# Performance work log

Measured on AMD Instinct MI355X. Metric: run time of the kernel, lower is better.

Reference implementation:

```python
import jax, jax.numpy as jnp
import numpy as np

N_NODES = 50000
N_EDGES = 800000
D_IN = 128
D_OUT = 128


def setup_inputs() -> dict:
    key = jax.random.key(0)
    ks = jax.random.split(key, 10)
    x = jax.random.normal(ks[0], (N_NODES, D_IN), dtype=jnp.float32)
    src = jax.random.randint(ks[1], (N_EDGES,), 0, N_NODES, dtype=jnp.int32)
    dst = jax.random.randint(ks[2], (N_EDGES,), 0, N_NODES, dtype=jnp.int32)
    s = 1.0 / np.sqrt(D_IN)
    def lin(k, din, dout):
        kw, kb = jax.random.split(k)
        W = jax.random.uniform(kw, (din, dout), minval=-s, maxval=s, dtype=jnp.float32)
        b = jax.random.uniform(kb, (dout,), minval=-s, maxval=s, dtype=jnp.float32)
        return W, b
    W1, b1 = lin(ks[3], D_IN, D_IN)
    W2, b2 = lin(ks[4], D_IN, D_IN)
    W3, b3 = lin(ks[5], D_IN, D_OUT)
    return dict(x=x, W1=W1, b1=b1, W2=W2, b2=b2, W3=W3, b3=b3, src=src, dst=dst)


def reference(x, W1, b1, W2, b2, W3, b3, src, dst):
    n = x.shape[0]
    ones = jnp.ones(src.shape[0], dtype=x.dtype)
    in_deg = jax.ops.segment_sum(ones, dst, num_segments=n)    # [N]
    out_deg = jax.ops.segment_sum(ones, src, num_segments=n)   # [N]

    def sage_gcn(h, W, b):
        # DGL SAGEConv(aggregator_type='gcn'), eval mode (feat_drop = identity):
        # h_neigh = (sum_{j in N(i)} h_j + h_i) / (in_deg_i + 1); out = h_neigh @ W + b
        neigh = jax.ops.segment_sum(h[src], dst, num_segments=n)  # [N, D]
        h_neigh = (neigh + h) / (in_deg + 1.0)[:, None]
        return h_neigh @ W + b

    h = sage_gcn(x, W1, b1)
    h = sage_gcn(h, W2, b2)

    # DGL GraphConv norm='both', allow_zero_in_degree=True:
    # out = D_in^{-1/2} A D_out^{-1/2} h W + b, degrees clamped to >= 1
    norm_out = jnp.clip(out_deg, 1.0) ** -0.5
    norm_in = jnp.clip(in_deg, 1.0) ** -0.5
    hs = h * norm_out[:, None]
    agg = jax.ops.segment_sum(hs[src], dst, num_segments=n)
    out = (agg * norm_in[:, None]) @ W3 + b3
    return out
```

## Files before the change

kernel.cpp:

```cpp
#include <hip/hip_runtime.h>

#define NN 50000
#define NE 800000
#define D 128

#define CH 32
#define EPC (NE / CH)
#define RGH 4
#define NPRH (NN / RGH)
#define CSRCAP (NE + 16 * NN)

typedef short bf16x8 __attribute__((ext_vector_type(8)));
typedef float f32x4 __attribute__((ext_vector_type(4)));


__device__ __forceinline__ unsigned bf16rne(float f) {
  unsigned u = __float_as_uint(f);
  return (u + 0x7fffu + ((u >> 16) & 1u)) >> 16;
}
__device__ __forceinline__ unsigned packbf(float lo, float hi) {
  return bf16rne(lo) | (bf16rne(hi) << 16);
}

__global__ __launch_bounds__(256) void cvtw_kernel(const float* __restrict__ x,
                                                   const float* __restrict__ W1,
                                                   const float* __restrict__ W2,
                                                   const float* __restrict__ W3,
                                                   unsigned short* __restrict__ hbf,
                                                   unsigned short* __restrict__ T1,
                                                   unsigned short* __restrict__ T2,
                                                   unsigned short* __restrict__ T3) {
  int b = blockIdx.x;
  int tid = threadIdx.x;
  if (b < 6250) {
    int i = b * 256 + tid;
    float4 v = ((const float4*)x)[i];
    uint2 p;
    p.x = packbf(v.x, v.y);
    p.y = packbf(v.z, v.w);
    ((uint2*)hbf)[i] = p;
  } else if (b < 6442) {
    int g = b - 6250;
    int w = g >> 6;
    int i = (g & 63) * 256 + tid;
    const float* W = (w == 0) ? W1 : (w == 1) ? W2 : W3;
    unsigned short* T = (w == 0) ? T1 : (w == 1) ? T2 : T3;
    int n = i >> 7, k = i & 127;
    T[n * 128 + k] = (unsigned short)bf16rne(W[k * 128 + n]);
  } else {
    if (tid < 16) ((uint4*)(hbf + (size_t)NN * D))[tid] = make_uint4(0, 0, 0, 0);
  }
}

__global__ __launch_bounds__(1024) void hist_kernel(const int* __restrict__ src,
                                                    const int* __restrict__ dst,
                                                    int* __restrict__ partial_dst,
                                                    int* __restrict__ partial_src) {
  __shared__ int hd[NPRH];
  __shared__ int hs[NPRH];
  int tid = threadIdx.x;
  int c = blockIdx.x >> 2;
  int r = blockIdx.x & 3;
  int base = r * NPRH;
  for (int i = tid; i < NPRH; i += 1024) { hd[i] = 0; hs[i] = 0; }
  __syncthreads();
  int e0 = c * EPC;
  for (int i = tid; i < EPC; i += 1024) {
    int d = dst[e0 + i];
    int s = src[e0 + i];
    unsigned dr = (unsigned)(d - base);
    unsigned sr = (unsigned)(s - base);
    if (dr < NPRH) atomicAdd(&hd[dr], 1);
    if (sr < NPRH) atomicAdd(&hs[sr], 1);
  }
  __syncthreads();
  for (int i = tid; i < NPRH; i += 1024) {
    partial_dst[c * NN + base + i] = hd[i];
    partial_src[c * NN + base + i] = hs[i];
  }
}

__device__ __forceinline__ int block_excl_scan(int v, int* wsum) {
  int lane = threadIdx.x & 63;
  int w = threadIdx.x >> 6;
  int incl = v;
#pragma unroll
  for (int off = 1; off < 64; off <<= 1) {
    int t = __shfl_up(incl, off);
    if (lane >= off) incl += t;
  }
  if (lane == 63) wsum[w] = incl;
  __syncthreads();
  int wo = 0;
#pragma unroll
  for (int j = 0; j < 4; ++j)
    if (j < w) wo += wsum[j];
  return wo + incl - v;
}

__global__ __launch_bounds__(256) void degscan_kernel(int* __restrict__ partial_dst,
                                                      const int* __restrict__ partial_src,
                                                      int* __restrict__ degtmp,
                                                      int* __restrict__ deg_out,
                                                      int* __restrict__ row_ptr,
                                                      int* __restrict__ partials, int N) {
  __shared__ int wsum[4];
  int d = blockIdx.x * 256 + threadIdx.x;
  int run = 0;
  if (d < N) {
#pragma unroll
    for (int c = 0; c < CH; ++c) {
      int v = partial_dst[c * NN + d];
      partial_dst[c * NN + d] = run;
      run += v;
    }
    degtmp[d] = run;
    int ro = 0;
#pragma unroll
    for (int c = 0; c < CH; ++c) ro += partial_src[c * NN + d];
    deg_out[d] = ro;
  }
  int pad = (run + 15) & ~15;
  int excl = block_excl_scan(pad, wsum);
  if (d < N) row_ptr[d] = excl;
  if (threadIdx.x == 255) partials[blockIdx.x] = excl + pad;
}

__global__ __launch_bounds__(256) void scan2(int* __restrict__ partials,
                                             int* __restrict__ row_ptr, int nb, int N) {
  __shared__ int wsum[4];
  int v = (threadIdx.x < nb) ? partials[threadIdx.x] : 0;
  int excl = block_excl_scan(v, wsum);
  if (threadIdx.x < nb) partials[threadIdx.x] = excl;
  if (threadIdx.x == nb - 1) row_ptr[N] = excl + v;
}

__global__ __launch_bounds__(256) void scan3(int* __restrict__ row_ptr,
                                             const int* __restrict__ partials, int N) {
  int i = blockIdx.x * 256 + threadIdx.x;
  if (i < N) row_ptr[i] += partials[blockIdx.x];
}

__global__ __launch_bounds__(1024) void fill_kernel(const int* __restrict__ src,
                                                    const int* __restrict__ dst,
                                                    const int* __restrict__ row_ptr,
                                                    const int* __restrict__ partial_dst,
                                                    int* __restrict__ csr_src) {
  __shared__ int cur[NPRH];
  int tid = threadIdx.x;
  int c = blockIdx.x >> 2;
  int r = blockIdx.x & 3;
  int base = r * NPRH;
  for (int i = tid; i < NPRH; i += 1024)
    cur[i] = row_ptr[base + i] + partial_dst[c * NN + base + i];
  __syncthreads();
  int e0 = c * EPC;
  for (int i = tid; i < EPC; i += 1024) {
    int d = dst[e0 + i];
    unsigned dr = (unsigned)(d - base);
    if (dr < NPRH) {
      int pos = atomicAdd(&cur[dr], 1);
      csr_src[pos] = src[e0 + i];
    }
  }
}

__global__ __launch_bounds__(256) void pad_kernel(const int* __restrict__ row_ptr,
                                                  const int* __restrict__ degtmp,
                                                  int* __restrict__ csr_src, int N) {
  int i = blockIdx.x * 256 + threadIdx.x;
  if (i >= N) return;
  int s = row_ptr[i] + degtmp[i];
  int e = row_ptr[i + 1];
  for (int j = s; j < e; ++j) csr_src[j] = NN;
}

__device__ __forceinline__ void bacc(float* a, uint4 u) {
  a[0] += __uint_as_float(u.x << 16);
  a[1] += __uint_as_float(u.x & 0xffff0000u);
  a[2] += __uint_as_float(u.y << 16);
  a[3] += __uint_as_float(u.y & 0xffff0000u);
  a[4] += __uint_as_float(u.z << 16);
  a[5] += __uint_as_float(u.z & 0xffff0000u);
  a[6] += __uint_as_float(u.w << 16);
  a[7] += __uint_as_float(u.w & 0xffff0000u);
}

template <int MODE>
__global__ __launch_bounds__(256, 8) void agg_kernel(const unsigned short* __restrict__ hb,
                                                     const int* __restrict__ row_ptr,
                                                     const int* __restrict__ csr_src,
                                                     const int* __restrict__ degtmp,
                                                     unsigned short* __restrict__ outb, int N) {
  int wid = blockIdx.x * 4 + (threadIdx.x >> 6);
  int lane = threadIdx.x & 63;
  if (wid >= N) return;
  int start = row_ptr[wid];
  int iters = (row_ptr[wid + 1] - start) >> 4;
  int indeg = degtmp[wid];
  int q = lane >> 4;
  int col = lane & 15;
  uint4 sr = make_uint4(0, 0, 0, 0);
  if (MODE == 0) sr = ((const uint4*)(hb + (size_t)wid * D))[col];
  float a0[8] = {0, 0, 0, 0, 0, 0, 0, 0};
  float a1[8] = {0, 0, 0, 0, 0, 0, 0, 0};
  const int* ce = csr_src + start + q;
  for (int it = 0; it < iters; ++it, ce += 16) {
    int i0 = ce[0];
    int i1 = ce[4];
    int i2 = ce[8];
    int i3 = ce[12];
    uint4 u0 = ((const uint4*)(hb + (size_t)i0 * D))[col];
    uint4 u1 = ((const uint4*)(hb + (size_t)i1 * D))[col];
    uint4 u2 = ((const uint4*)(hb + (size_t)i2 * D))[col];
    uint4 u3 = ((const uint4*)(hb + (size_t)i3 * D))[col];
    bacc(a0, u0);
    bacc(a1, u1);
    bacc(a0, u2);
    bacc(a1, u3);
  }
#pragma unroll
  for (int j = 0; j < 8; ++j) a0[j] += a1[j];
#pragma unroll
  for (int j = 0; j < 8; ++j) {
    a0[j] += __shfl_xor(a0[j], 16);
    a0[j] += __shfl_xor(a0[j], 32);
  }
  if (MODE == 0) {
    float sf[8] = {0, 0, 0, 0, 0, 0, 0, 0};
    bacc(sf, sr);
    float inv = 1.0f / (float)(indeg + 1);
#pragma unroll
    for (int j = 0; j < 8; ++j) a0[j] = (a0[j] + sf[j]) * inv;
  } else {
    float sc = rsqrtf(fmaxf((float)indeg, 1.0f));
#pragma unroll
    for (int j = 0; j < 8; ++j) a0[j] *= sc;
  }
  if (q == 0) {
    uint4 p;
    p.x = packbf(a0[0], a0[1]);
    p.y = packbf(a0[2], a0[3]);
    p.z = packbf(a0[4], a0[5]);
    p.w = packbf(a0[6], a0[7]);
    ((uint4*)(outb + (size_t)wid * D))[col] = p;
  }
}

template <int MODE, int OUT_BF>
__global__ __launch_bounds__(256) void mgemm_kernel(const unsigned short* __restrict__ A,
                                                    const unsigned short* __restrict__ WT,
                                                    const float* __restrict__ bias,
                                                    const int* __restrict__ deg_out,
                                                    float* __restrict__ outf,
                                                    unsigned short* __restrict__ outb, int N) {
  __shared__ unsigned short sWT[128 * 136];
  int tid = threadIdx.x;
  for (int g = tid; g < 2048; g += 256) {
    int n = g >> 4, c = g & 15;
    uint4 v = ((const uint4*)WT)[g];
    *(uint4*)&sWT[n * 136 + c * 8] = v;
  }
  int wv = tid >> 6;
  int lane = tid & 63;
  int q = lane >> 4;
  int ln = lane & 15;
  int row0 = blockIdx.x * 64 + wv * 16;
  int arow = row0 + ln;
  if (arow >= N) arow = 0;
  const unsigned short* Ar = A + (size_t)arow * 128 + q * 8;
  bf16x8 af0 = *(const bf16x8*)(Ar + 0);
  bf16x8 af1 = *(const bf16x8*)(Ar + 32);
  bf16x8 af2 = *(const bf16x8*)(Ar + 64);
  bf16x8 af3 = *(const bf16x8*)(Ar + 96);
  f32x4 acc[8];
#pragma unroll
  for (int t = 0; t < 8; ++t) acc[t] = (f32x4){0.f, 0.f, 0.f, 0.f};
  __syncthreads();
#pragma unroll
  for (int t = 0; t < 8; ++t) {
    const unsigned short* Wr = &sWT[(t * 16 + ln) * 136 + q * 8];
    bf16x8 b0 = *(const bf16x8*)(Wr + 0);
    bf16x8 b1 = *(const bf16x8*)(Wr + 32);
    bf16x8 b2 = *(const bf16x8*)(Wr + 64);
    bf16x8 b3 = *(const bf16x8*)(Wr + 96);
    acc[t] = __builtin_amdgcn_mfma_f32_16x16x32_bf16(af0, b0, acc[t], 0, 0, 0);
    acc[t] = __builtin_amdgcn_mfma_f32_16x16x32_bf16(af1, b1, acc[t], 0, 0, 0);
    acc[t] = __builtin_amdgcn_mfma_f32_16x16x32_bf16(af2, b2, acc[t], 0, 0, 0);
    acc[t] = __builtin_amdgcn_mfma_f32_16x16x32_bf16(af3, b3, acc[t], 0, 0, 0);
  }
  float scl[4];
#pragma unroll
  for (int r = 0; r < 4; ++r) {
    scl[r] = 1.0f;
    if (MODE == 1) {
      int row = row0 + q * 4 + r;
      int rr = (row < N) ? row : 0;
      scl[r] = rsqrtf(fmaxf((float)deg_out[rr], 1.0f));
    }
  }
#pragma unroll
  for (int t = 0; t < 8; ++t) {
    float b = bias[t * 16 + ln];
#pragma unroll
    for (int r = 0; r < 4; ++r) {
      int row = row0 + q * 4 + r;
      if (row < N) {
        float v = (acc[t][r] + b) * scl[r];
        if (OUT_BF)
          outb[(size_t)row * 128 + t * 16 + ln] = (unsigned short)bf16rne(v);
        else
          outf[(size_t)row * 128 + t * 16 + ln] = v;
      }
    }
  }
}


extern "C" void kernel_launch(void* const* d_in, const int* in_sizes, int n_in,
                              void* d_out, int out_size, void* d_ws, size_t ws_size,
                              hipStream_t stream) {
  const float* x = (const float*)d_in[0];
  const float* W1 = (const float*)d_in[1];
  const float* b1 = (const float*)d_in[2];
  const float* W2 = (const float*)d_in[3];
  const float* b2 = (const float*)d_in[4];
  const float* W3 = (const float*)d_in[5];
  const float* b3 = (const float*)d_in[6];
  const int* src = (const int*)d_in[7];
  const int* dst = (const int*)d_in[8];
  float* out = (float*)d_out;

  const int N = NN;

  unsigned short* hbf = (unsigned short*)d_ws;
  unsigned short* aggB = hbf + (size_t)(NN + 1) * D;
  unsigned short* WT1 = aggB + (size_t)NN * D;
  unsigned short* WT2 = WT1 + D * D;
  unsigned short* WT3 = WT2 + D * D;
  int* partial_dst = (int*)(WT3 + D * D);
  int* partial_src = partial_dst + (size_t)CH * NN;
  int* degtmp = partial_src + (size_t)CH * NN;
  int* deg_out = degtmp + NN;
  int* row_ptr = deg_out + NN;
  int* partials = row_ptr + NN + 1;
  int* csr_src = partials + 256;

  const int scanBlocks = (N + 255) / 256;

  cvtw_kernel<<<6443, 256, 0, stream>>>(x, W1, W2, W3, hbf, WT1, WT2, WT3);
  hist_kernel<<<CH * RGH, 1024, 0, stream>>>(src, dst, partial_dst, partial_src);
  degscan_kernel<<<scanBlocks, 256, 0, stream>>>(partial_dst, partial_src, degtmp,
                                                 deg_out, row_ptr, partials, N);
  scan2<<<1, 256, 0, stream>>>(partials, row_ptr, scanBlocks, N);
  scan3<<<scanBlocks, 256, 0, stream>>>(row_ptr, partials, N);
  fill_kernel<<<CH * RGH, 1024, 0, stream>>>(src, dst, row_ptr, partial_dst, csr_src);
  pad_kernel<<<scanBlocks, 256, 0, stream>>>(row_ptr, degtmp, csr_src, N);

  int aggBlocks = (N + 3) / 4;
  int gemmBlocks = (N + 63) / 64;

  agg_kernel<0><<<aggBlocks, 256, 0, stream>>>(hbf, row_ptr, csr_src, degtmp, aggB, N);
  mgemm_kernel<0, 1><<<gemmBlocks, 256, 0, stream>>>(aggB, WT1, b1, deg_out, nullptr, hbf, N);
  agg_kernel<0><<<aggBlocks, 256, 0, stream>>>(hbf, row_ptr, csr_src, degtmp, aggB, N);
  mgemm_kernel<1, 1><<<gemmBlocks, 256, 0, stream>>>(aggB, WT2, b2, deg_out, nullptr, hbf, N);
  agg_kernel<1><<<aggBlocks, 256, 0, stream>>>(hbf, row_ptr, csr_src, degtmp, aggB, N);
  mgemm_kernel<0, 0><<<gemmBlocks, 256, 0, stream>>>(aggB, WT3, b3, deg_out, out, nullptr, N);
}
```

Baseline: 268.4 us.

## Fuse preprocessing kernels, pad rows to 4, assign 16-lane group per node

Merges the conversion and histogram kernels into one launch. It drops the scan3 and pad kernels by having fill_kernel and agg_kernel add the block partial offsets themselves, and fill_kernel now writes the padding entries. CSR row padding shrinks from 16 to 4 entries, which cuts wasted gathers of the zero row. Aggregation now gives each node one 16-lane group instead of a 64-lane wave, which removes the cross-lane shuffle reduction but leaves each group walking its neighbours serially. The aim is fewer kernel launches and less padding work, at the cost of less memory-level parallelism per node.

New measurement: 260.9 us. -2.8%, faster.

```diff
diff --git a/kernel.cpp b/kernel.cpp
--- a/kernel.cpp
+++ b/kernel.cpp
@@ -10,6 +10,10 @@
 #define NPRH (NN / RGH)
 #define CSRCAP (NE + 16 * NN)
 
+#define HIST_BLOCKS (CH * RGH)
+#define CVT_BLOCKS 1563
+#define WT_BLOCKS 48
+
 typedef short bf16x8 __attribute__((ext_vector_type(8)));
 typedef float f32x4 __attribute__((ext_vector_type(4)));
 
@@ -22,61 +26,56 @@
   return bf16rne(lo) | (bf16rne(hi) << 16);
 }
 
-__global__ __launch_bounds__(256) void cvtw_kernel(const float* __restrict__ x,
-                                                   const float* __restrict__ W1,
-                                                   const float* __restrict__ W2,
-                                                   const float* __restrict__ W3,
-                                                   unsigned short* __restrict__ hbf,
-                                                   unsigned short* __restrict__ T1,
-                                                   unsigned short* __restrict__ T2,
-                                                   unsigned short* __restrict__ T3) {
+__global__ __launch_bounds__(1024) void cvtw_hist_kernel(
+    const float* __restrict__ x, const float* __restrict__ W1,
+    const float* __restrict__ W2, const float* __restrict__ W3,
+    unsigned short* __restrict__ hbf, unsigned short* __restrict__ T1,
+    unsigned short* __restrict__ T2, unsigned short* __restrict__ T3,
+    const int* __restrict__ src, const int* __restrict__ dst,
+    int* __restrict__ partial_dst, int* __restrict__ partial_src) {
+  __shared__ int hd[NPRH];
+  __shared__ int hs[NPRH];
   int b = blockIdx.x;
   int tid = threadIdx.x;
-  if (b < 6250) {
-    int i = b * 256 + tid;
-    float4 v = ((const float4*)x)[i];
-    uint2 p;
-    p.x = packbf(v.x, v.y);
-    p.y = packbf(v.z, v.w);
-    ((uint2*)hbf)[i] = p;
-  } else if (b < 6442) {
-    int g = b - 6250;
-    int w = g >> 6;
-    int i = (g & 63) * 256 + tid;
+  if (b < HIST_BLOCKS) {
+    int c = b >> 2;
+    int r = b & 3;
+    int base = r * NPRH;
+    for (int i = tid; i < NPRH; i += 1024) { hd[i] = 0; hs[i] = 0; }
+    __syncthreads();
+    int e0 = c * EPC;
+    for (int i = tid; i < EPC; i += 1024) {
+      int d = dst[e0 + i];
+      int s = src[e0 + i];
+      unsigned dr = (unsigned)(d - base);
+      unsigned sr = (unsigned)(s - base);
+      if (dr < NPRH) atomicAdd(&hd[dr], 1);
+      if (sr < NPRH) atomicAdd(&hs[sr], 1);
+    }
+    __syncthreads();
+    for (int i = tid; i < NPRH; i += 1024) {
+      partial_dst[c * NN + base + i] = hd[i];
+      partial_src[c * NN + base + i] = hs[i];
+    }
+  } else if (b < HIST_BLOCKS + CVT_BLOCKS) {
+    int i = (b - HIST_BLOCKS) * 1024 + tid;
+    if (i < NN * D / 4) {
+      float4 v = ((const float4*)x)[i];
+      uint2 p;
+      p.x = packbf(v.x, v.y);
+      p.y = packbf(v.z, v.w);
+      ((uint2*)hbf)[i] = p;
+    }
+  } else if (b < HIST_BLOCKS + CVT_BLOCKS + WT_BLOCKS) {
+    int g = b - (HIST_BLOCKS + CVT_BLOCKS);
+    int w = g >> 4;
+    int i = (g & 15) * 1024 + tid;
     const float* W = (w == 0) ? W1 : (w == 1) ? W2 : W3;
     unsigned short* T = (w == 0) ? T1 : (w == 1) ? T2 : T3;
     int n = i >> 7, k = i & 127;
     T[n * 128 + k] = (unsigned short)bf16rne(W[k * 128 + n]);
   } else {
     if (tid < 16) ((uint4*)(hbf + (size_t)NN * D))[tid] = make_uint4(0, 0, 0, 0);
-  }
-}
-
-__global__ __launch_bounds__(1024) void hist_kernel(const int* __restrict__ src,
-                                                    const int* __restrict__ dst,
-                                                    int* __restrict__ partial_dst,
-                                                    int* __restrict__ partial_src) {
-  __shared__ int hd[NPRH];
-  __shared__ int hs[NPRH];
-  int tid = threadIdx.x;
-  int c = blockIdx.x >> 2;
-  int r = blockIdx.x & 3;
-  int base = r * NPRH;
-  for (int i = tid; i < NPRH; i += 1024) { hd[i] = 0; hs[i] = 0; }
-  __syncthreads();
-  int e0 = c * EPC;
-  for (int i = tid; i < EPC; i += 1024) {
-    int d = dst[e0 + i];
-    int s = src[e0 + i];
-    unsigned dr = (unsigned)(d - base);
-    unsigned sr = (unsigned)(s - base);
-    if (dr < NPRH) atomicAdd(&hd[dr], 1);
-    if (sr < NPRH) atomicAdd(&hs[sr], 1);
-  }
-  __syncthreads();
-  for (int i = tid; i < NPRH; i += 1024) {
-    partial_dst[c * NN + base + i] = hd[i];
-    partial_src[c * NN + base + i] = hs[i];
   }
 }
 
@@ -120,30 +119,23 @@
     for (int c = 0; c < CH; ++c) ro += partial_src[c * NN + d];
     deg_out[d] = ro;
   }
-  int pad = (run + 15) & ~15;
+  int pad = (run + 3) & ~3;
   int excl = block_excl_scan(pad, wsum);
-  if (d < N) row_ptr[d] = excl;
+  if (d <= N) row_ptr[d] = excl;
   if (threadIdx.x == 255) partials[blockIdx.x] = excl + pad;
 }
 
-__global__ __launch_bounds__(256) void scan2(int* __restrict__ partials,
-                                             int* __restrict__ row_ptr, int nb, int N) {
+__global__ __launch_bounds__(256) void scan2(int* __restrict__ partials, int nb) {
   __shared__ int wsum[4];
   int v = (threadIdx.x < nb) ? partials[threadIdx.x] : 0;
   int excl = block_excl_scan(v, wsum);
   if (threadIdx.x < nb) partials[threadIdx.x] = excl;
-  if (threadIdx.x == nb - 1) row_ptr[N] = excl + v;
-}
-
-__global__ __launch_bounds__(256) void scan3(int* __restrict__ row_ptr,
-                                             const int* __restrict__ partials, int N) {
-  int i = blockIdx.x * 256 + threadIdx.x;
-  if (i < N) row_ptr[i] += partials[blockIdx.x];
 }
 
 __global__ __launch_bounds__(1024) void fill_kernel(const int* __restrict__ src,
                                                     const int* __restrict__ dst,
                                                     const int* __restrict__ row_ptr,
+                                                    const int* __restrict__ partials,
                                                     const int* __restrict__ partial_dst,
                                                     int* __restrict__ csr_src) {
   __shared__ int cur[NPRH];
@@ -151,8 +143,10 @@
   int c = blockIdx.x >> 2;
   int r = blockIdx.x & 3;
   int base = r * NPRH;
-  for (int i = tid; i < NPRH; i += 1024)
-    cur[i] = row_ptr[base + i] + partial_dst[c * NN + base + i];
+  for (int i = tid; i < NPRH; i += 1024) {
+    int nd = base + i;
+    cur[i] = row_ptr[nd] + partials[nd >> 8] + partial_dst[c * NN + nd];
+  }
   __syncthreads();
   int e0 = c * EPC;
   for (int i = tid; i < EPC; i += 1024) {
@@ -163,16 +157,15 @@
       csr_src[pos] = src[e0 + i];
     }
   }
-}
-
-__global__ __launch_bounds__(256) void pad_kernel(const int* __restrict__ row_ptr,
-                                                  const int* __restrict__ degtmp,
-                                                  int* __restrict__ csr_src, int N) {
-  int i = blockIdx.x * 256 + threadIdx.x;
-  if (i >= N) return;
-  int s = row_ptr[i] + degtmp[i];
-  int e = row_ptr[i + 1];
-  for (int j = s; j < e; ++j) csr_src[j] = NN;
+  if (c == CH - 1) {
+    __syncthreads();
+    for (int i = tid; i < NPRH; i += 1024) {
+      int nd = base + i;
+      int s = cur[i];
+      int e = row_ptr[nd + 1] + partials[(nd + 1) >> 8];
+      for (int j = s; j < e; ++j) csr_src[j] = NN;
+    }
+  }
 }
 
 __device__ __forceinline__ void bacc(float* a, uint4 u) {
@@ -189,31 +182,29 @@
 template <int MODE>
 __global__ __launch_bounds__(256, 8) void agg_kernel(const unsigned short* __restrict__ hb,
                                                      const int* __restrict__ row_ptr,
+                                                     const int* __restrict__ partials,
                                                      const int* __restrict__ csr_src,
                                                      const int* __restrict__ degtmp,
                                                      unsigned short* __restrict__ outb, int N) {
-  int wid = blockIdx.x * 4 + (threadIdx.x >> 6);
-  int lane = threadIdx.x & 63;
-  if (wid >= N) return;
-  int start = row_ptr[wid];
-  int iters = (row_ptr[wid + 1] - start) >> 4;
-  int indeg = degtmp[wid];
-  int q = lane >> 4;
-  int col = lane & 15;
-  uint4 sr = make_uint4(0, 0, 0, 0);
-  if (MODE == 0) sr = ((const uint4*)(hb + (size_t)wid * D))[col];
+  int qw = threadIdx.x >> 4;
+  int col = threadIdx.x & 15;
+  int node = blockIdx.x * 16 + qw;
+  if (node >= N) return;
+  int start = row_ptr[node] + partials[node >> 8];
+  int end = row_ptr[node + 1] + partials[(node + 1) >> 8];
+  int indeg = degtmp[node];
+  uint4 srow = make_uint4(0, 0, 0, 0);
+  if (MODE == 0) srow = ((const uint4*)(hb + (size_t)node * D))[col];
   float a0[8] = {0, 0, 0, 0, 0, 0, 0, 0};
   float a1[8] = {0, 0, 0, 0, 0, 0, 0, 0};
-  const int* ce = csr_src + start + q;
-  for (int it = 0; it < iters; ++it, ce += 16) {
-    int i0 = ce[0];
-    int i1 = ce[4];
-    int i2 = ce[8];
-    int i3 = ce[12];
-    uint4 u0 = ((const uint4*)(hb + (size_t)i0 * D))[col];
-    uint4 u1 = ((const uint4*)(hb + (size_t)i1 * D))[col];
-    uint4 u2 = ((const uint4*)(hb + (size_t)i2 * D))[col];
-    uint4 u3 = ((const uint4*)(hb + (size_t)i3 * D))[col];
+  const int* ce = csr_src + start;
+  int cnt = end - start;
+  for (int it = 0; it < cnt; it += 4) {
+    int4 ix = *(const int4*)(ce + it);
+    uint4 u0 = ((const uint4*)(hb + (size_t)ix.x * D))[col];
+    uint4 u1 = ((const uint4*)(hb + (size_t)ix.y * D))[col];
+    uint4 u2 = ((const uint4*)(hb + (size_t)ix.z * D))[col];
+    uint4 u3 = ((const uint4*)(hb + (size_t)ix.w * D))[col];
     bacc(a0, u0);
     bacc(a1, u1);
     bacc(a0, u2);
@@ -221,14 +212,9 @@
   }
 #pragma unroll
   for (int j = 0; j < 8; ++j) a0[j] += a1[j];
-#pragma unroll
-  for (int j = 0; j < 8; ++j) {
-    a0[j] += __shfl_xor(a0[j], 16);
-    a0[j] += __shfl_xor(a0[j], 32);
-  }
   if (MODE == 0) {
     float sf[8] = {0, 0, 0, 0, 0, 0, 0, 0};
-    bacc(sf, sr);
+    bacc(sf, srow);
     float inv = 1.0f / (float)(indeg + 1);
 #pragma unroll
     for (int j = 0; j < 8; ++j) a0[j] = (a0[j] + sf[j]) * inv;
@@ -237,14 +223,12 @@
 #pragma unroll
     for (int j = 0; j < 8; ++j) a0[j] *= sc;
   }
-  if (q == 0) {
-    uint4 p;
-    p.x = packbf(a0[0], a0[1]);
-    p.y = packbf(a0[2], a0[3]);
-    p.z = packbf(a0[4], a0[5]);
-    p.w = packbf(a0[6], a0[7]);
-    ((uint4*)(outb + (size_t)wid * D))[col] = p;
-  }
+  uint4 p;
+  p.x = packbf(a0[0], a0[1]);
+  p.y = packbf(a0[2], a0[3]);
+  p.z = packbf(a0[4], a0[5]);
+  p.w = packbf(a0[6], a0[7]);
+  ((uint4*)(outb + (size_t)node * D))[col] = p;
 }
 
 template <int MODE, int OUT_BF>
@@ -348,22 +332,24 @@
 
   const int scanBlocks = (N + 255) / 256;
 
-  cvtw_kernel<<<6443, 256, 0, stream>>>(x, W1, W2, W3, hbf, WT1, WT2, WT3);
-  hist_kernel<<<CH * RGH, 1024, 0, stream>>>(src, dst, partial_dst, partial_src);
+  cvtw_hist_kernel<<<HIST_BLOCKS + CVT_BLOCKS + WT_BLOCKS + 1, 1024, 0, stream>>>(
+      x, W1, W2, W3, hbf, WT1, WT2, WT3, src, dst, partial_dst, partial_src);
   degscan_kernel<<<scanBlocks, 256, 0, stream>>>(partial_dst, partial_src, degtmp,
                                                  deg_out, row_ptr, partials, N);
-  scan2<<<1, 256, 0, stream>>>(partials, row_ptr, scanBlocks, N);
-  scan3<<<scanBlocks, 256, 0, stream>>>(row_ptr, partials, N);
-  fill_kernel<<<CH * RGH, 1024, 0, stream>>>(src, dst, row_ptr, partial_dst, csr_src);
-  pad_kernel<<<scanBlocks, 256, 0, stream>>>(row_ptr, degtmp, csr_src, N);
-
-  int aggBlocks = (N + 3) / 4;
+  scan2<<<1, 256, 0, stream>>>(partials, scanBlocks);
+  fill_kernel<<<CH * RGH, 1024, 0, stream>>>(src, dst, row_ptr, partials, partial_dst,
+                                             csr_src);
+
+  int aggBlocks = (N + 15) / 16;
   int gemmBlocks = (N + 63) / 64;
 
-  agg_kernel<0><<<aggBlocks, 256, 0, stream>>>(hbf, row_ptr, csr_src, degtmp, aggB, N);
+  agg_kernel<0><<<aggBlocks, 256, 0, stream>>>(hbf, row_ptr, partials, csr_src, degtmp,
+                                               aggB, N);
   mgemm_kernel<0, 1><<<gemmBlocks, 256, 0, stream>>>(aggB, WT1, b1, deg_out, nullptr, hbf, N);
-  agg_kernel<0><<<aggBlocks, 256, 0, stream>>>(hbf, row_ptr, csr_src, degtmp, aggB, N);
+  agg_kernel<0><<<aggBlocks, 256, 0, stream>>>(hbf, row_ptr, partials, csr_src, degtmp,
+                                               aggB, N);
   mgemm_kernel<1, 1><<<gemmBlocks, 256, 0, stream>>>(aggB, WT2, b2, deg_out, nullptr, hbf, N);
-  agg_kernel<1><<<aggBlocks, 256, 0, stream>>>(hbf, row_ptr, csr_src, degtmp, aggB, N);
+  agg_kernel<1><<<aggBlocks, 256, 0, stream>>>(hbf, row_ptr, partials, csr_src, degtmp,
+                                               aggB, N);
   mgemm_kernel<0, 0><<<gemmBlocks, 256, 0, stream>>>(aggB, WT3, b3, deg_out, out, nullptr, N);
 }
```
